# Optimization experiments

Measured on AMD Instinct MI355X. Metric: run time of the kernel, lower is better.

## Reference

```python
import jax, jax.numpy as jnp
import numpy as np

C = 64  # chunk size, fixed in the original module


def setup_inputs() -> dict:
    key = jax.random.key(0)
    k1, k2, k3, k4, k5 = jax.random.split(key, 5)
    B, T, D, H = 4, 4096, 1024, 8
    out = jax.random.normal(k1, (B, T, D), jnp.float32)
    W_write = jax.random.normal(k2, (D, D), jnp.float32) * 0.02
    # original inits proj_read to zeros; use small random weight so the memory path is exercised
    W_read = jax.random.normal(k3, (D, D), jnp.float32) * 0.02
    W_beta = jax.random.normal(k4, (H, D), jnp.float32) * 0.02
    decay = 4.6 + jax.random.normal(k5, (H,), jnp.float32) * 0.1
    return {"out": out, "W_write": W_write, "W_read": W_read, "W_beta": W_beta, "decay": decay}


def reference(out, W_write, W_read, W_beta, decay):
    B, T, D = out.shape
    H = decay.shape[0]
    d = D // H
    assert T % C == 0  # chosen shapes avoid padding (pad_len == 0 path)
    N = T // C

    x = out.astype(jnp.float32)
    xh = x.reshape(B, T, H, d)
    rk = xh / jnp.maximum(jnp.linalg.norm(xh, axis=-1, keepdims=True), 1e-12)
    rk = rk.transpose(0, 2, 1, 3)                                   # (B,H,T,d) read keys
    wk = jnp.pad(rk[:, :, :-1], ((0, 0), (0, 0), (1, 0), (0, 0)))    # write keys = shifted read keys
    v = (x @ W_write.T).reshape(B, T, H, d).transpose(0, 2, 1, 3)    # (B,H,T,d)
    beta = jax.nn.sigmoid(x @ W_beta.T).transpose(0, 2, 1)[..., None]  # (B,H,T,1)
    v = v * beta
    wk_beta = wk * beta

    log_gamma = jnp.log(jax.nn.sigmoid(decay))                       # (H,)
    pos = jnp.arange(C, dtype=jnp.float32)
    cum_decay = (pos + 1.0) * log_gamma[:, None]                     # (H,C)
    tril = jnp.tril(jnp.ones((C, C), jnp.float32))
    L_mask = jnp.exp((cum_decay[:, :, None] - cum_decay[:, None, :]) * tril) * tril  # (H,C,C)
    decay_exp = jnp.exp(cum_decay)[:, :, None]                       # (H,C,1)
    chunk_total = jnp.exp(cum_decay[:, -1])[:, None, None]           # (H,1,1)
    dw = jnp.exp(cum_decay[:, -1:] - cum_decay)[:, :, None]          # (H,C,1)

    rk_c = rk.reshape(B, H, N, C, d)
    wk_c = wk.reshape(B, H, N, C, d)
    v_c = v.reshape(B, H, N, C, d)
    wkb_c = wk_beta.reshape(B, H, N, C, d)

    # UT transform: A = strictly-lower part of -(beta K)(K^T) with decay, then forward substitution
    strict_lower = jnp.tril(jnp.ones((C, C), bool), -1)
    A = -(wkb_c @ jnp.swapaxes(wk_c, -1, -2)) * L_mask[None, :, None]
    A = jnp.where(strict_lower, A, 0.0)

    def ut_body(i, A):
        row = A[..., i, :]                                           # (B,H,N,C)
        new_row = row + jnp.einsum('bhnj,bhnjk->bhnk', row, A)
        return A.at[..., i, :].set(new_row)

    A = jax.lax.fori_loop(1, C, ut_body, A)
    A = A + jnp.eye(C, dtype=A.dtype)

    v_c = A @ v_c
    wk_cum = A @ (wkb_c * decay_exp[None, :, None])

    # cross-chunk state recurrence
    causal = jnp.tril(jnp.ones((C, C), bool))                        # keep diag + lower
    xs = (jnp.moveaxis(rk_c, 2, 0), jnp.moveaxis(wk_c, 2, 0),
          jnp.moveaxis(v_c, 2, 0), jnp.moveaxis(wk_cum, 2, 0))
    S0 = jnp.zeros((B, H, d, d), jnp.float32)

    def chunk_step(S, xs_i):
        rk_i, wk_i, v_i, wkc_i = xs_i                                # each (B,H,C,d)
        attn = (rk_i @ jnp.swapaxes(wk_i, -1, -2)) * L_mask[None]
        attn = jnp.where(causal, attn, 0.0)
        v_new = v_i - wkc_i @ S
        o_i = (rk_i * decay_exp[None]) @ S + attn @ v_new
        S_new = chunk_total[None] * S + jnp.swapaxes(wk_i * dw[None], -1, -2) @ v_new
        return S_new, o_i

    _, o = jax.lax.scan(chunk_step, S0, xs)                          # (N,B,H,C,d)
    o = jnp.moveaxis(o, 0, 2).reshape(B, H, T, d).transpose(0, 2, 1, 3).reshape(B, T, D)
    return out + (o @ W_read.T).astype(out.dtype)
```

## Files before the change

kernel.cpp:

```cpp
#include <hip/hip_runtime.h>
#include <hip/hip_bf16.h>
#include <math.h>


#define T_LEN 4096
typedef unsigned short ushort;
typedef __attribute__((ext_vector_type(2))) unsigned short us2;
typedef __attribute__((ext_vector_type(4))) unsigned short us4;
typedef __attribute__((ext_vector_type(8))) unsigned short us8;
typedef __attribute__((ext_vector_type(8))) short short8v;
typedef __attribute__((ext_vector_type(4))) float f32x4;

__device__ __forceinline__ float bf2f(ushort u) {
  union { unsigned int u; float f; } c; c.u = ((unsigned int)u) << 16; return c.f;
}
__device__ __forceinline__ ushort f2bf(float x) {
  union { float f; unsigned int u; } c; c.f = x;
  unsigned int u = c.u + 0x7FFFu + ((c.u >> 16) & 1u);
  return (ushort)(u >> 16);
}
__device__ __forceinline__ ushort f2bf_fast(float x) {
  __hip_bfloat16 h = __float2bfloat16(x);
  return *reinterpret_cast<ushort*>(&h);
}

__global__ __launch_bounds__(128) void k_prep(
    const float* __restrict__ x, const float* __restrict__ Wb,
    ushort* __restrict__ rk, float* __restrict__ beta)
{
  int bt = blockIdx.x;
  int b = bt >> 12, t = bt & 4095;
  int tid = threadIdx.x;
  __shared__ float xs[1024];
  __shared__ float red[16];
  {
    const float4* x4 = (const float4*)(x + (size_t)bt * 1024);
    float4* xs4 = (float4*)xs;
    xs4[tid] = x4[tid];
    xs4[tid + 128] = x4[tid + 128];
  }
  __syncthreads();
  int h = tid >> 4;
  int e0 = h * 128 + (tid & 15) * 8;
  float ss = 0.f;
  #pragma unroll
  for (int s = 0; s < 8; ++s) { float v = xs[e0 + s]; ss += v * v; }
  #pragma unroll
  for (int m = 1; m < 16; m <<= 1) ss += __shfl_xor(ss, m, 64);
  float inv = 1.f / fmaxf(sqrtf(ss), 1e-12f);
  {
    int bh = b * 8 + h;
    us8 o;
    #pragma unroll
    for (int s = 0; s < 8; ++s) o[s] = f2bf(xs[e0 + s] * inv);
    *(us8*)(rk + ((size_t)bh * T_LEN + t) * 128 + (tid & 15) * 8) = o;
  }
  const float* xk = xs + tid * 8;
  #pragma unroll
  for (int h2 = 0; h2 < 8; ++h2) {
    const float* wb = Wb + (size_t)h2 * 1024 + tid * 8;
    float p = 0.f;
    #pragma unroll
    for (int s = 0; s < 8; ++s) p += xk[s] * wb[s];
    #pragma unroll
    for (int m = 1; m < 64; m <<= 1) p += __shfl_xor(p, m, 64);
    if ((tid & 63) == 0) red[(tid >> 6) * 8 + h2] = p;
  }
  __syncthreads();
  if (tid < 8) {
    float s = red[tid] + red[8 + tid];
    beta[((size_t)(b * 8 + tid)) * T_LEN + t] = 1.f / (1.f + expf(-s));
  }
}

#define LDK 40
template<int MODE>
__global__ __launch_bounds__(256) void k_gemm(
    const void* __restrict__ Am_, const float* __restrict__ W,
    const float* __restrict__ beta, const float* __restrict__ xadd,
    void* __restrict__ out_)
{
  __shared__ ushort As[128 * LDK];
  __shared__ ushort Bs[128 * LDK];
  const int n0 = blockIdx.x * 128;
  const int m0 = blockIdx.y * 128;
  const int tid = threadIdx.x;
  const int lane = tid & 63;
  const int wid = tid >> 6;
  const int wr = wid >> 1, wc = wid & 1;
  const int c = lane & 15, g = lane >> 4;
  const int srow = tid >> 2;
  const int seg = tid & 3;

  f32x4 acc[4][4] = {};

  for (int k0 = 0; k0 < 1024; k0 += 32) {
    if (MODE == 0) {
      const float* a0 = (const float*)Am_ + (size_t)(m0 + srow) * 1024 + k0 + seg * 8;
      const float* a1 = (const float*)Am_ + (size_t)(m0 + srow + 64) * 1024 + k0 + seg * 8;
      float4 p0 = *(const float4*)a0, p1 = *(const float4*)(a0 + 4);
      float4 q0 = *(const float4*)a1, q1 = *(const float4*)(a1 + 4);
      us8 o0, o1;
      o0[0]=f2bf_fast(p0.x); o0[1]=f2bf_fast(p0.y); o0[2]=f2bf_fast(p0.z); o0[3]=f2bf_fast(p0.w);
      o0[4]=f2bf_fast(p1.x); o0[5]=f2bf_fast(p1.y); o0[6]=f2bf_fast(p1.z); o0[7]=f2bf_fast(p1.w);
      o1[0]=f2bf_fast(q0.x); o1[1]=f2bf_fast(q0.y); o1[2]=f2bf_fast(q0.z); o1[3]=f2bf_fast(q0.w);
      o1[4]=f2bf_fast(q1.x); o1[5]=f2bf_fast(q1.y); o1[6]=f2bf_fast(q1.z); o1[7]=f2bf_fast(q1.w);
      *(us8*)&As[srow * LDK + seg * 8] = o0;
      *(us8*)&As[(srow + 64) * LDK + seg * 8] = o1;
    } else {
      us8 o0 = *(const us8*)((const ushort*)Am_ + (size_t)(m0 + srow) * 1024 + k0 + seg * 8);
      us8 o1 = *(const us8*)((const ushort*)Am_ + (size_t)(m0 + srow + 64) * 1024 + k0 + seg * 8);
      *(us8*)&As[srow * LDK + seg * 8] = o0;
      *(us8*)&As[(srow + 64) * LDK + seg * 8] = o1;
    }
    {
      const float* b0 = W + (size_t)(n0 + srow) * 1024 + k0 + seg * 8;
      const float* b1 = W + (size_t)(n0 + srow + 64) * 1024 + k0 + seg * 8;
      float4 p0 = *(const float4*)b0, p1 = *(const float4*)(b0 + 4);
      float4 q0 = *(const float4*)b1, q1 = *(const float4*)(b1 + 4);
      us8 o0, o1;
      o0[0]=f2bf_fast(p0.x); o0[1]=f2bf_fast(p0.y); o0[2]=f2bf_fast(p0.z); o0[3]=f2bf_fast(p0.w);
      o0[4]=f2bf_fast(p1.x); o0[5]=f2bf_fast(p1.y); o0[6]=f2bf_fast(p1.z); o0[7]=f2bf_fast(p1.w);
      o1[0]=f2bf_fast(q0.x); o1[1]=f2bf_fast(q0.y); o1[2]=f2bf_fast(q0.z); o1[3]=f2bf_fast(q0.w);
      o1[4]=f2bf_fast(q1.x); o1[5]=f2bf_fast(q1.y); o1[6]=f2bf_fast(q1.z); o1[7]=f2bf_fast(q1.w);
      *(us8*)&Bs[srow * LDK + seg * 8] = o0;
      *(us8*)&Bs[(srow + 64) * LDK + seg * 8] = o1;
    }
    __syncthreads();
    short8v af[4], bf[4];
    #pragma unroll
    for (int mi = 0; mi < 4; ++mi)
      af[mi] = *(const short8v*)&As[(wr * 64 + mi * 16 + c) * LDK + g * 8];
    #pragma unroll
    for (int ni = 0; ni < 4; ++ni)
      bf[ni] = *(const short8v*)&Bs[(wc * 64 + ni * 16 + c) * LDK + g * 8];
    #pragma unroll
    for (int mi = 0; mi < 4; ++mi)
      #pragma unroll
      for (int ni = 0; ni < 4; ++ni)
        acc[mi][ni] = __builtin_amdgcn_mfma_f32_16x16x32_bf16(af[mi], bf[ni], acc[mi][ni], 0, 0, 0);
    __syncthreads();
  }

  if (MODE == 0) {
    ushort* vb = (ushort*)out_;
    const int hh = n0 >> 7;
    #pragma unroll
    for (int mi = 0; mi < 4; ++mi) {
      #pragma unroll
      for (int ni = 0; ni < 4; ++ni) {
        int jc = wc * 64 + ni * 16 + c;
        #pragma unroll
        for (int j = 0; j < 4; ++j) {
          int m = m0 + wr * 64 + mi * 16 + g * 4 + j;
          int b = m >> 12, t = m & 4095;
          size_t base = (size_t)(b * 8 + hh) * T_LEN + t;
          float bv = beta[base];
          vb[base * 128 + jc] = f2bf(acc[mi][ni][j] * bv);
        }
      }
    }
  } else {
    float* out = (float*)out_;
    #pragma unroll
    for (int mi = 0; mi < 4; ++mi) {
      #pragma unroll
      for (int ni = 0; ni < 4; ++ni) {
        int n = n0 + wc * 64 + ni * 16 + c;
        #pragma unroll
        for (int j = 0; j < 4; ++j) {
          int m = m0 + wr * 64 + mi * 16 + g * 4 + j;
          size_t idx = (size_t)m * 1024 + n;
          out[idx] = xadd[idx] + acc[mi][ni][j];
        }
      }
    }
  }
}

__global__ __launch_bounds__(256) void k_chunk(
    const ushort* __restrict__ rk, ushort* __restrict__ vb,
    ushort* __restrict__ wkcum, ushort* __restrict__ attn,
    const float* __restrict__ beta, const float* __restrict__ decay,
    ushort* __restrict__ wkdwT)
{
  int bh = blockIdx.x >> 6;
  int n = blockIdx.x & 63;
  int h = bh & 7;
  int tid = threadIdx.x;
  int lane = tid & 63, w = tid >> 6;
  int c = lane & 15, g = lane >> 4;

  __shared__ __align__(16) char smem[39952];
  ushort* rkb  = (ushort*)smem;
  float*  redp = (float*)smem;
  ushort* Ab1  = (ushort*)smem;
  ushort* Ab2  = (ushort*)(smem + 9216);
  float*  Af   = (float*)(smem + 21760);
  ushort* xT   = (ushort*)(smem + 18432);
  float*  gpow  = (float*)(smem + 39168);
  float*  betaS = (float*)(smem + 39432);
  float*  bd    = (float*)(smem + 39688);

  float lg = logf(1.f / (1.f + expf(-decay[h])));
  if (tid < 65) gpow[tid] = expf(lg * (float)tid);
  if (tid < 64) betaS[tid] = beta[(size_t)bh * T_LEN + n * 64 + tid];
  const int t0 = n * 64;
  const size_t bhbase = (size_t)bh * T_LEN;
  const us8 zero8 = {0, 0, 0, 0, 0, 0, 0, 0};

  #pragma unroll
  for (int u = 0; u < 5; ++u) {
    int idx = tid + u * 256;
    int row = idx >> 4, cb = idx & 15;
    us8 v = zero8;
    int t = t0 + row - 1;
    if (row <= 64 && t >= 0) v = *(const us8*)(rk + (bhbase + t) * 128 + cb * 8);
    *(us8*)&rkb[row * 136 + cb * 8] = v;
  }
  for (int idx = tid; idx < 64 * 68; idx += 256) Af[idx] = 0.f;
  __syncthreads();
  if (tid < 64) bd[tid] = betaS[tid] * gpow[tid + 1];

  const size_t abase = ((size_t)bh * 64 + n) * 4096;
  {
    const int TR[14] = {0,1,1,2,2,2,3,3,3,3,4,4,4,4};
    const int TC[14] = {0,0,1,0,1,2,0,1,2,3,0,1,2,3};
    #pragma unroll
    for (int ti = 0; ti < 14; ++ti) {
      if ((ti & 3) != w) continue;
      const int tr = TR[ti], tc = TC[ti];
      f32x4 acc = {0.f, 0.f, 0.f, 0.f};
      #pragma unroll
      for (int ks = 0; ks < 4; ++ks) {
        short8v a = *(const short8v*)&rkb[(tr * 16 + c) * 136 + ks * 32 + g * 8];
        short8v b = *(const short8v*)&rkb[(tc * 16 + c) * 136 + ks * 32 + g * 8];
        acc = __builtin_amdgcn_mfma_f32_16x16x32_bf16(a, b, acc, 0, 0, 0);
      }
      #pragma unroll
      for (int r = 0; r < 4; ++r) {
        int a_ = tr * 16 + g * 4 + r;
        int j = tc * 16 + c;
        float val = acc[r];
        if (a_ <= 63) Af[a_ * 68 + j] = (a_ > j) ? (-betaS[a_] * val * gpow[a_ - j]) : 0.f;
        if (a_ >= 1 && a_ <= 64) {
          if (j <= a_ - 1)      attn[abase + (size_t)(a_ - 1) * 64 + j] = f2bf(val * gpow[a_ - 1 - j]);
          else if (a_ <= 63)    attn[abase + (size_t)(a_ - 1) * 64 + j] = 0;
        }
      }
    }
  }
  {
    const int ZR[6] = {0,0,0,1,1,2};
    const int ZC[6] = {1,2,3,2,3,3};
    int rr = tid >> 4, cc2 = tid & 15;
    #pragma unroll
    for (int z = 0; z < 6; ++z) {
      int r_att = ZR[z] * 16 - 1 + rr;
      if (r_att >= 0) attn[abase + (size_t)r_att * 64 + ZC[z] * 16 + cc2] = 0;
    }
  }
  __syncthreads();

  {
    int k = tid & 63, sp = tid >> 6;
    for (int i = 1; i < 64; ++i) {
      float part = 0.f;
      #pragma unroll
      for (int jj = 0; jj < 16; ++jj) {
        int j = sp * 16 + jj;
        part += Af[i * 68 + j] * Af[j * 68 + k];
      }
      redp[sp * 64 + k] = part;
      __syncthreads();
      if (tid < 64) Af[i * 68 + tid] += redp[tid] + redp[64 + tid] + redp[128 + tid] + redp[192 + tid];
      __syncthreads();
    }
  }
  {
    int i = tid >> 2, j0 = (tid & 3) * 16;
    #pragma unroll
    for (int jj = 0; jj < 16; ++jj) {
      int j = j0 + jj;
      float av = Af[i * 68 + j] + ((i == j) ? 1.f : 0.f);
      Ab1[i * 72 + j] = f2bf(av * bd[j]);
      Ab2[i * 72 + j] = f2bf(av);
    }
  }
  __syncthreads();

  #pragma unroll
  for (int u = 0; u < 4; ++u) {
    int idx = tid + u * 256;
    int j = idx & 63, eb = idx >> 6;
    int t = t0 + j - 1;
    us8 v = zero8;
    if (t >= 0) v = *(const us8*)(rk + (bhbase + t) * 128 + eb * 8);
    #pragma unroll
    for (int s = 0; s < 8; ++s) xT[(eb * 8 + s) * 72 + j] = v[s];
  }
  __syncthreads();

  {
    f32x4 acc[8] = {};
    #pragma unroll
    for (int ks = 0; ks < 2; ++ks) {
      short8v a = *(const short8v*)&Ab1[(w * 16 + c) * 72 + ks * 32 + g * 8];
      #pragma unroll
      for (int nt = 0; nt < 8; ++nt) {
        short8v b = *(const short8v*)&xT[(nt * 16 + c) * 72 + ks * 32 + g * 8];
        acc[nt] = __builtin_amdgcn_mfma_f32_16x16x32_bf16(a, b, acc[nt], 0, 0, 0);
      }
    }
    #pragma unroll
    for (int nt = 0; nt < 8; ++nt)
      #pragma unroll
      for (int r = 0; r < 4; ++r) {
        int i = w * 16 + g * 4 + r, e = nt * 16 + c;
        wkcum[(bhbase + t0 + i) * 128 + e] = f2bf(acc[nt][r]);
      }
  }
  {
    const size_t kbase = ((size_t)bh * 64 + n) * 8192;
    #pragma unroll
    for (int u = 0; u < 4; ++u) {
      int idx = tid + u * 256;
      int e = idx >> 3, seg = idx & 7;
      us8 v = *(const us8*)&xT[e * 72 + seg * 8];
      us8 o;
      #pragma unroll
      for (int s = 0; s < 8; ++s) o[s] = f2bf(bf2f(v[s]) * gpow[63 - (seg * 8 + s)]);
      *(us8*)(wkdwT + kbase + (size_t)e * 64 + seg * 8) = o;
    }
  }
  __syncthreads();
  #pragma unroll
  for (int u = 0; u < 4; ++u) {
    int idx = tid + u * 256;
    int j = idx & 63, eb = idx >> 6;
    us8 v = *(const us8*)(vb + (bhbase + t0 + j) * 128 + eb * 8);
    #pragma unroll
    for (int s = 0; s < 8; ++s) xT[(eb * 8 + s) * 72 + j] = v[s];
  }
  __syncthreads();
  {
    f32x4 acc[8] = {};
    #pragma unroll
    for (int ks = 0; ks < 2; ++ks) {
      short8v a = *(const short8v*)&Ab2[(w * 16 + c) * 72 + ks * 32 + g * 8];
      #pragma unroll
      for (int nt = 0; nt < 8; ++nt) {
        short8v b = *(const short8v*)&xT[(nt * 16 + c) * 72 + ks * 32 + g * 8];
        acc[nt] = __builtin_amdgcn_mfma_f32_16x16x32_bf16(a, b, acc[nt], 0, 0, 0);
      }
    }
    #pragma unroll
    for (int nt = 0; nt < 8; ++nt)
      #pragma unroll
      for (int r = 0; r < 4; ++r) {
        int i = w * 16 + g * 4 + r, e = nt * 16 + c;
        vb[(bhbase + t0 + i) * 128 + e] = f2bf(acc[nt][r]);
      }
  }
}

#define SCAN_STEP(W_, R_, T_, K_, V_, nW, nR, nT, nK, nV, n_) {                 \
  const int t0s = (n_) * 64;                                                    \
  { const int np = ((n_) < 63) ? (n_) + 1 : 63;                                 \
    const size_t rb = (bhbase + (size_t)(np * 64 + 16 * w + c)) * 128;          \
    _Pragma("unroll")                                                           \
    for (int ks = 0; ks < 4; ++ks) {                                            \
      nW[ks] = *(const short8v*)(wkcum + rb + ks * 32 + g * 8);                 \
      nR[ks] = *(const short8v*)(rk    + rb + ks * 32 + g * 8); }               \
    const size_t ab = ((size_t)bh * 64 + np) * 4096 + (size_t)(16 * w + c) * 64;\
    nT[0] = *(const short8v*)(attn + ab + g * 8);                               \
    nT[1] = *(const short8v*)(attn + ab + 32 + g * 8);                          \
    const size_t kb = ((size_t)bh * 64 + np) * 8192;                            \
    nK[0] = *(const short8v*)(wkdwT + kb + (size_t)(32 * w + c) * 64 + g * 8);  \
    nK[1] = *(const short8v*)(wkdwT + kb + (size_t)(32 * w + c) * 64 + 32 + g * 8); \
    nK[2] = *(const short8v*)(wkdwT + kb + (size_t)(32 * w + 16 + c) * 64 + g * 8); \
    nK[3] = *(const short8v*)(wkdwT + kb + (size_t)(32 * w + 16 + c) * 64 + 32 + g * 8); \
    _Pragma("unroll")                                                           \
    for (int r = 0; r < 4; ++r)                                                 \
      nV[r] = vb[(bhbase + (size_t)(np * 64 + 16 * w + 4 * g + r)) * 128 + q0 + c]; } \
  f32x4 accA = {}, accB = {};                                                   \
  _Pragma("unroll")                                                             \
  for (int ks = 0; ks < 4; ++ks) {                                              \
    short8v b0 = *(const short8v*)&ST[c * 136 + ks * 32 + g * 8];               \
    accA = __builtin_amdgcn_mfma_f32_16x16x32_bf16(W_[ks], b0, accA, 0, 0, 0);  \
    accB = __builtin_amdgcn_mfma_f32_16x16x32_bf16(R_[ks], b0, accB, 0, 0, 0); }\
  _Pragma("unroll")                                                             \
  for (int r = 0; r < 4; ++r) {                                                 \
    int i = 16 * w + 4 * g + r;                                                 \
    accB[r] *= gB[r];                                                           \
    vnL[c * 72 + i] = f2bf(bf2f(V_[r]) - accA[r]); }                            \
  asm volatile("s_waitcnt lgkmcnt(0)" ::: "memory");                            \
  __builtin_amdgcn_s_barrier();                                                 \
  short8v vf0 = *(const short8v*)&vnL[c * 72 + g * 8];                          \
  short8v vf1 = *(const short8v*)&vnL[c * 72 + 32 + g * 8];                     \
  accB = __builtin_amdgcn_mfma_f32_16x16x32_bf16(T_[0], vf0, accB, 0, 0, 0);    \
  accB = __builtin_amdgcn_mfma_f32_16x16x32_bf16(T_[1], vf1, accB, 0, 0, 0);    \
  _Pragma("unroll")                                                             \
  for (int r = 0; r < 4; ++r) {                                                 \
    int i = 16 * w + 4 * g + r;                                                 \
    og[((size_t)b_ * T_LEN + t0s + i) * 1024 + h * 128 + q0 + c] = f2bf(accB[r]); } \
  _Pragma("unroll")                                                             \
  for (int r = 0; r < 4; ++r) { accS0[r] *= ct; accS1[r] *= ct; }               \
  accS0 = __builtin_amdgcn_mfma_f32_16x16x32_bf16(K_[0], vf0, accS0, 0, 0, 0);  \
  accS0 = __builtin_amdgcn_mfma_f32_16x16x32_bf16(K_[1], vf1, accS0, 0, 0, 0);  \
  accS1 = __builtin_amdgcn_mfma_f32_16x16x32_bf16(K_[2], vf0, accS1, 0, 0, 0);  \
  accS1 = __builtin_amdgcn_mfma_f32_16x16x32_bf16(K_[3], vf1, accS1, 0, 0, 0);  \
  _Pragma("unroll")                                                             \
  for (int r = 0; r < 4; ++r) {                                                 \
    int p0r = 32 * w + 4 * g + r;                                               \
    ST[c * 136 + p0r]      = f2bf(accS0[r]);                                    \
    ST[c * 136 + p0r + 16] = f2bf(accS1[r]); }                                  \
  asm volatile("s_waitcnt lgkmcnt(0)" ::: "memory");                            \
  __builtin_amdgcn_s_barrier();                                                 \
}

__global__ __launch_bounds__(256) void k_scan_fused(
    const ushort* __restrict__ rk, const ushort* __restrict__ vb,
    const ushort* __restrict__ wkcum, const ushort* __restrict__ attn,
    const ushort* __restrict__ wkdwT, const float* __restrict__ decay,
    ushort* __restrict__ og)
{
  const int bh = blockIdx.x & 31;
  const int q0 = (blockIdx.x >> 5) * 16;
  const int b_ = bh >> 3, h = bh & 7;
  const int tid = threadIdx.x;
  const int lane = tid & 63, w = tid >> 6;
  const int c = lane & 15, g = lane >> 4;

  __shared__ ushort ST[16 * 136];
  __shared__ ushort vnL[16 * 72];
  __shared__ float gpow[65];

  float lg = logf(1.f / (1.f + expf(-decay[h])));
  if (tid < 65) gpow[tid] = expf(lg * (float)tid);
  for (int idx = tid; idx < 16 * 136; idx += 256) ST[idx] = 0;
  __syncthreads();
  const float ct = gpow[64];
  float gB[4];
  #pragma unroll
  for (int r = 0; r < 4; ++r) gB[r] = gpow[16 * w + 4 * g + r + 1];
  const size_t bhbase = (size_t)bh * T_LEN;

  f32x4 accS0 = {}, accS1 = {};
  short8v aW[4], aR[4], aT[2], aK[4];
  short8v bW[4], bR[4], bT[2], bK[4];
  ushort aV[4], bV[4];
  {
    const size_t rb = (bhbase + (size_t)(16 * w + c)) * 128;
    #pragma unroll
    for (int ks = 0; ks < 4; ++ks) {
      aW[ks] = *(const short8v*)(wkcum + rb + ks * 32 + g * 8);
      aR[ks] = *(const short8v*)(rk + rb + ks * 32 + g * 8);
    }
    const size_t ab = (size_t)bh * 64 * 4096 + (size_t)(16 * w + c) * 64;
    aT[0] = *(const short8v*)(attn + ab + g * 8);
    aT[1] = *(const short8v*)(attn + ab + 32 + g * 8);
    const size_t kb = (size_t)bh * 64 * 8192;
    aK[0] = *(const short8v*)(wkdwT + kb + (size_t)(32 * w + c) * 64 + g * 8);
    aK[1] = *(const short8v*)(wkdwT + kb + (size_t)(32 * w + c) * 64 + 32 + g * 8);
    aK[2] = *(const short8v*)(wkdwT + kb + (size_t)(32 * w + 16 + c) * 64 + g * 8);
    aK[3] = *(const short8v*)(wkdwT + kb + (size_t)(32 * w + 16 + c) * 64 + 32 + g * 8);
    #pragma unroll
    for (int r = 0; r < 4; ++r)
      aV[r] = vb[(bhbase + (size_t)(16 * w + 4 * g + r)) * 128 + q0 + c];
  }
  for (int n = 0; n < 64; n += 2) {
    SCAN_STEP(aW, aR, aT, aK, aV, bW, bR, bT, bK, bV, n);
    SCAN_STEP(bW, bR, bT, bK, bV, aW, aR, aT, aK, aV, n + 1);
  }
}

extern "C" void kernel_launch(void* const* d_in, const int* in_sizes, int n_in,
                              void* d_out, int out_size, void* d_ws, size_t ws_size,
                              hipStream_t stream) {
  const float* x   = (const float*)d_in[0];
  const float* Ww  = (const float*)d_in[1];
  const float* Wr  = (const float*)d_in[2];
  const float* Wb  = (const float*)d_in[3];
  const float* dec = (const float*)d_in[4];
  float* out = (float*)d_out;
  ushort* ws = (ushort*)d_ws;
  const size_t SZ = 16777216ull;
  ushort* rk    = ws;
  ushort* vb    = ws + SZ;
  ushort* wkcum = ws + 2 * SZ;
  ushort* og    = ws + 3 * SZ;
  ushort* attn  = ws + 4 * SZ;
  float*  beta  = (float*)(ws + 4 * SZ + 8388608ull);
  ushort* wkdwT = ws + 4 * SZ + 8388608ull + 262144ull;
  const size_t NEED = (4 * SZ + 8388608ull + 262144ull + SZ) * 2ull;
  if (ws_size < NEED) {
    hipMemcpyAsync(d_out, (const void*)x, (size_t)out_size * 4, hipMemcpyDeviceToDevice, stream);
    return;
  }

  k_prep<<<dim3(16384), dim3(128), 0, stream>>>(x, Wb, rk, beta);
  k_gemm<0><<<dim3(8, 128), dim3(256), 0, stream>>>((const void*)x, Ww, beta, nullptr, (void*)vb);
  k_chunk<<<dim3(2048), dim3(256), 0, stream>>>(rk, vb, wkcum, attn, beta, dec, wkdwT);
  k_scan_fused<<<dim3(256), dim3(256), 0, stream>>>(rk, vb, wkcum, attn, wkdwT, dec, og);
  k_gemm<1><<<dim3(8, 128), dim3(256), 0, stream>>>((const void*)og, Wr, nullptr, (const float*)x, (void*)out);
}
```

Before: 426.1 us.

## Pre-convert GEMM operands to bf16 and split scan over 8-column slices

```diff
diff --git a/kernel.cpp b/kernel.cpp
--- a/kernel.cpp
+++ b/kernel.cpp
@@ -19,14 +19,27 @@
   unsigned int u = c.u + 0x7FFFu + ((c.u >> 16) & 1u);
   return (ushort)(u >> 16);
 }
-__device__ __forceinline__ ushort f2bf_fast(float x) {
-  __hip_bfloat16 h = __float2bfloat16(x);
-  return *reinterpret_cast<ushort*>(&h);
+
+__global__ __launch_bounds__(256) void k_wcvt(
+    const float* __restrict__ Ww, const float* __restrict__ Wr,
+    ushort* __restrict__ Wwb, ushort* __restrict__ Wrb)
+{
+  size_t i = ((size_t)blockIdx.x * 256 + threadIdx.x) * 8;
+  float4 p0 = *(const float4*)(Ww + i), p1 = *(const float4*)(Ww + i + 4);
+  us8 o;
+  o[0]=f2bf(p0.x); o[1]=f2bf(p0.y); o[2]=f2bf(p0.z); o[3]=f2bf(p0.w);
+  o[4]=f2bf(p1.x); o[5]=f2bf(p1.y); o[6]=f2bf(p1.z); o[7]=f2bf(p1.w);
+  *(us8*)(Wwb + i) = o;
+  float4 q0 = *(const float4*)(Wr + i), q1 = *(const float4*)(Wr + i + 4);
+  us8 o2;
+  o2[0]=f2bf(q0.x); o2[1]=f2bf(q0.y); o2[2]=f2bf(q0.z); o2[3]=f2bf(q0.w);
+  o2[4]=f2bf(q1.x); o2[5]=f2bf(q1.y); o2[6]=f2bf(q1.z); o2[7]=f2bf(q1.w);
+  *(us8*)(Wrb + i) = o2;
 }
 
 __global__ __launch_bounds__(128) void k_prep(
     const float* __restrict__ x, const float* __restrict__ Wb,
-    ushort* __restrict__ rk, float* __restrict__ beta)
+    ushort* __restrict__ rk, float* __restrict__ beta, ushort* __restrict__ xb)
 {
   int bt = blockIdx.x;
   int b = bt >> 12, t = bt & 4095;
@@ -55,6 +68,12 @@
     for (int s = 0; s < 8; ++s) o[s] = f2bf(xs[e0 + s] * inv);
     *(us8*)(rk + ((size_t)bh * T_LEN + t) * 128 + (tid & 15) * 8) = o;
   }
+  {
+    us8 o;
+    #pragma unroll
+    for (int s = 0; s < 8; ++s) o[s] = f2bf(xs[tid * 8 + s]);
+    *(us8*)(xb + (size_t)bt * 1024 + tid * 8) = o;
+  }
   const float* xk = xs + tid * 8;
   #pragma unroll
   for (int h2 = 0; h2 < 8; ++h2) {
@@ -76,7 +95,7 @@
 #define LDK 40
 template<int MODE>
 __global__ __launch_bounds__(256) void k_gemm(
-    const void* __restrict__ Am_, const float* __restrict__ W,
+    const ushort* __restrict__ A, const ushort* __restrict__ Wb,
     const float* __restrict__ beta, const float* __restrict__ xadd,
     void* __restrict__ out_)
 {
@@ -95,34 +114,15 @@
   f32x4 acc[4][4] = {};
 
   for (int k0 = 0; k0 < 1024; k0 += 32) {
-    if (MODE == 0) {
-      const float* a0 = (const float*)Am_ + (size_t)(m0 + srow) * 1024 + k0 + seg * 8;
-      const float* a1 = (const float*)Am_ + (size_t)(m0 + srow + 64) * 1024 + k0 + seg * 8;
-      float4 p0 = *(const float4*)a0, p1 = *(const float4*)(a0 + 4);
-      float4 q0 = *(const float4*)a1, q1 = *(const float4*)(a1 + 4);
-      us8 o0, o1;
-      o0[0]=f2bf_fast(p0.x); o0[1]=f2bf_fast(p0.y); o0[2]=f2bf_fast(p0.z); o0[3]=f2bf_fast(p0.w);
-      o0[4]=f2bf_fast(p1.x); o0[5]=f2bf_fast(p1.y); o0[6]=f2bf_fast(p1.z); o0[7]=f2bf_fast(p1.w);
-      o1[0]=f2bf_fast(q0.x); o1[1]=f2bf_fast(q0.y); o1[2]=f2bf_fast(q0.z); o1[3]=f2bf_fast(q0.w);
-      o1[4]=f2bf_fast(q1.x); o1[5]=f2bf_fast(q1.y); o1[6]=f2bf_fast(q1.z); o1[7]=f2bf_fast(q1.w);
+    {
+      us8 o0 = *(const us8*)(A + (size_t)(m0 + srow) * 1024 + k0 + seg * 8);
+      us8 o1 = *(const us8*)(A + (size_t)(m0 + srow + 64) * 1024 + k0 + seg * 8);
       *(us8*)&As[srow * LDK + seg * 8] = o0;
       *(us8*)&As[(srow + 64) * LDK + seg * 8] = o1;
-    } else {
-      us8 o0 = *(const us8*)((const ushort*)Am_ + (size_t)(m0 + srow) * 1024 + k0 + seg * 8);
-      us8 o1 = *(const us8*)((const ushort*)Am_ + (size_t)(m0 + srow + 64) * 1024 + k0 + seg * 8);
-      *(us8*)&As[srow * LDK + seg * 8] = o0;
-      *(us8*)&As[(srow + 64) * LDK + seg * 8] = o1;
     }
     {
-      const float* b0 = W + (size_t)(n0 + srow) * 1024 + k0 + seg * 8;
-      const float* b1 = W + (size_t)(n0 + srow + 64) * 1024 + k0 + seg * 8;
-      float4 p0 = *(const float4*)b0, p1 = *(const float4*)(b0 + 4);
-      float4 q0 = *(const float4*)b1, q1 = *(const float4*)(b1 + 4);
-      us8 o0, o1;
-      o0[0]=f2bf_fast(p0.x); o0[1]=f2bf_fast(p0.y); o0[2]=f2bf_fast(p0.z); o0[3]=f2bf_fast(p0.w);
-      o0[4]=f2bf_fast(p1.x); o0[5]=f2bf_fast(p1.y); o0[6]=f2bf_fast(p1.z); o0[7]=f2bf_fast(p1.w);
-      o1[0]=f2bf_fast(q0.x); o1[1]=f2bf_fast(q0.y); o1[2]=f2bf_fast(q0.z); o1[3]=f2bf_fast(q0.w);
-      o1[4]=f2bf_fast(q1.x); o1[5]=f2bf_fast(q1.y); o1[6]=f2bf_fast(q1.z); o1[7]=f2bf_fast(q1.w);
+      us8 o0 = *(const us8*)(Wb + (size_t)(n0 + srow) * 1024 + k0 + seg * 8);
+      us8 o1 = *(const us8*)(Wb + (size_t)(n0 + srow + 64) * 1024 + k0 + seg * 8);
       *(us8*)&Bs[srow * LDK + seg * 8] = o0;
       *(us8*)&Bs[(srow + 64) * LDK + seg * 8] = o1;
     }
@@ -382,7 +382,7 @@
     nK[3] = *(const short8v*)(wkdwT + kb + (size_t)(32 * w + 16 + c) * 64 + 32 + g * 8); \
     _Pragma("unroll")                                                           \
     for (int r = 0; r < 4; ++r)                                                 \
-      nV[r] = vb[(bhbase + (size_t)(np * 64 + 16 * w + 4 * g + r)) * 128 + q0 + c]; } \
+      nV[r] = vb[(bhbase + (size_t)(np * 64 + 16 * w + 4 * g + r)) * 128 + qc]; } \
   f32x4 accA = {}, accB = {};                                                   \
   _Pragma("unroll")                                                             \
   for (int ks = 0; ks < 4; ++ks) {                                              \
@@ -403,7 +403,8 @@
   _Pragma("unroll")                                                             \
   for (int r = 0; r < 4; ++r) {                                                 \
     int i = 16 * w + 4 * g + r;                                                 \
-    og[((size_t)b_ * T_LEN + t0s + i) * 1024 + h * 128 + q0 + c] = f2bf(accB[r]); } \
+    if (c < 8)                                                                  \
+      og[((size_t)b_ * T_LEN + t0s + i) * 1024 + h * 128 + q0 + c] = f2bf(accB[r]); } \
   _Pragma("unroll")                                                             \
   for (int r = 0; r < 4; ++r) { accS0[r] *= ct; accS1[r] *= ct; }               \
   accS0 = __builtin_amdgcn_mfma_f32_16x16x32_bf16(K_[0], vf0, accS0, 0, 0, 0);  \
@@ -426,11 +427,12 @@
     ushort* __restrict__ og)
 {
   const int bh = blockIdx.x & 31;
-  const int q0 = (blockIdx.x >> 5) * 16;
+  const int q0 = (blockIdx.x >> 5) * 8;
   const int b_ = bh >> 3, h = bh & 7;
   const int tid = threadIdx.x;
   const int lane = tid & 63, w = tid >> 6;
   const int c = lane & 15, g = lane >> 4;
+  const int qc = (q0 + c <= 127) ? (q0 + c) : 127;
 
   __shared__ ushort ST[16 * 136];
   __shared__ ushort vnL[16 * 72];
@@ -467,7 +469,7 @@
     aK[3] = *(const short8v*)(wkdwT + kb + (size_t)(32 * w + 16 + c) * 64 + 32 + g * 8);
     #pragma unroll
     for (int r = 0; r < 4; ++r)
-      aV[r] = vb[(bhbase + (size_t)(16 * w + 4 * g + r)) * 128 + q0 + c];
+      aV[r] = vb[(bhbase + (size_t)(16 * w + 4 * g + r)) * 128 + qc];
   }
   for (int n = 0; n < 64; n += 2) {
     SCAN_STEP(aW, aR, aT, aK, aV, bW, bR, bT, bK, bV, n);
@@ -493,15 +495,19 @@
   ushort* attn  = ws + 4 * SZ;
   float*  beta  = (float*)(ws + 4 * SZ + 8388608ull);
   ushort* wkdwT = ws + 4 * SZ + 8388608ull + 262144ull;
-  const size_t NEED = (4 * SZ + 8388608ull + 262144ull + SZ) * 2ull;
+  ushort* Wwb   = ws + 92536832ull;
+  ushort* Wrb   = ws + 93585408ull;
+  ushort* xb    = og;
+  const size_t NEED = 189267968ull;
   if (ws_size < NEED) {
     hipMemcpyAsync(d_out, (const void*)x, (size_t)out_size * 4, hipMemcpyDeviceToDevice, stream);
     return;
   }
 
-  k_prep<<<dim3(16384), dim3(128), 0, stream>>>(x, Wb, rk, beta);
-  k_gemm<0><<<dim3(8, 128), dim3(256), 0, stream>>>((const void*)x, Ww, beta, nullptr, (void*)vb);
+  k_wcvt<<<dim3(512), dim3(256), 0, stream>>>(Ww, Wr, Wwb, Wrb);
+  k_prep<<<dim3(16384), dim3(128), 0, stream>>>(x, Wb, rk, beta, xb);
+  k_gemm<0><<<dim3(8, 128), dim3(256), 0, stream>>>(xb, Wwb, beta, nullptr, (void*)vb);
   k_chunk<<<dim3(2048), dim3(256), 0, stream>>>(rk, vb, wkcum, attn, beta, dec, wkdwT);
-  k_scan_fused<<<dim3(256), dim3(256), 0, stream>>>(rk, vb, wkcum, attn, wkdwT, dec, og);
-  k_gemm<1><<<dim3(8, 128), dim3(256), 0, stream>>>((const void*)og, Wr, nullptr, (const float*)x, (void*)out);
-}
+  k_scan_fused<<<dim3(512), dim3(256), 0, stream>>>(rk, vb, wkcum, attn, wkdwT, dec, og);
+  k_gemm<1><<<dim3(8, 128), dim3(256), 0, stream>>>(og, Wrb, nullptr, (const float*)x, (void*)out);
+}
```

Result: slower. 489.2 us (+14.8%).
